# Optimization experiments

Measured on AMD Instinct MI355X. Metric: run time of the kernel, lower is better.

The kernel has to match this reference:

```python
import jax, jax.numpy as jnp
import numpy as np

T, X_D, M_N, CHUNK, REDUCE = 2048, 2048, 64, 64, 8
M_D = X_D // REDUCE          # 256
DECAY_D = M_D // 4           # 64
H_D = X_D * 2                # factor=2
FF_D = 256 * round(int(H_D * (2.0 / 3.0)) / 256)  # 2816


def setup_inputs() -> dict:
    key = jax.random.key(0)
    ks = jax.random.split(key, 20)
    def lin(k, out_d, in_d):
        return (jax.random.normal(k, (out_d, in_d), jnp.float32) / np.sqrt(in_d).astype(np.float32))
    return {
        "xs": jax.random.normal(ks[0], (T, X_D), jnp.float32),
        "attn_q": lin(ks[1], X_D // REDUCE, X_D),
        "attn_k": lin(ks[2], X_D // REDUCE, X_D // REDUCE),
        "attn_v": lin(ks[3], X_D, X_D),
        "attn_o": lin(ks[4], X_D, X_D),
        "attn_r": lin(ks[5], X_D, X_D),
        "mem_f": lin(ks[6], M_N, X_D),
        "mem_q": lin(ks[7], M_D, X_D),
        "mem_k": lin(ks[8], M_D, M_D),
        "mem_v": lin(ks[9], M_D, X_D),
        "mem_o": lin(ks[10], X_D, M_D),
        "mem_r": lin(ks[11], X_D, X_D),
        "mem_beta": -jnp.ones((M_N, M_D), jnp.float32),
        "mem_decay": 3.0 * jnp.ones((M_N, DECAY_D), jnp.float32),
        "mem_l": jax.random.uniform(ks[12], (M_N, M_D), dtype=jnp.float32),
        "ff_in1": lin(ks[13], FF_D, X_D),
        "ff_in2": lin(ks[14], FF_D, X_D),
        "ff_out": lin(ks[15], X_D, FF_D),
        "sn1_g": jnp.sqrt(jnp.float32(X_D)),
        "sn2_g": jnp.sqrt(jnp.float32(X_D)),
    }


def _rotate_half(x):
    x1 = x[..., ::2]
    x2 = x[..., 1::2]
    return jnp.stack((-x2, x1), axis=-1).reshape(x.shape)


def _scale_norm(x, g):
    return x * (g / (jnp.linalg.norm(x, axis=-1, keepdims=True) + 1e-8))


def _attn(xs, Wq, Wk, Wv, Wo, Wr):
    n = CHUNK
    q = xs @ Wq.T                       # (T, dk)
    k = q @ Wk.T                        # k is computed from q (as in source)
    v = xs @ Wv.T                       # (T, x_d)
    c = xs.shape[0] // n
    dk = q.shape[-1]
    q = q.reshape(c, n, dk)
    k = k.reshape(c, n, dk)
    v = v.reshape(c, n, v.shape[-1])

    def with_prev(a):                   # prepend previous chunk (zero for chunk 0)
        prev = jnp.concatenate([jnp.zeros_like(a[:1]), a[:-1]], axis=0)
        return jnp.concatenate([prev, a], axis=1)   # (c, 2n, d)

    k2, v2 = with_prev(k), with_prev(v)

    # RoPE over 2n key positions; queries take the last n positions
    inv_freq = 1.0 / (10000.0 ** (jnp.arange(0, dk, 2, dtype=jnp.float32) / dk))
    ang = jnp.arange(2 * n, dtype=jnp.float32)[:, None] * inv_freq[None, :]
    sin = jnp.repeat(jnp.sin(ang), 2, axis=-1)      # (2n, dk) interleaved
    cos = jnp.repeat(jnp.cos(ang), 2, axis=-1)
    q = q * cos[None, n:] + _rotate_half(q) * sin[None, n:]
    k2 = k2 * cos[None] + _rotate_half(k2) * sin[None]

    qk = jnp.einsum('cnk,cmk->cnm', q, k2) / jnp.sqrt(jnp.float32(dk))
    allowed = jnp.arange(2 * n)[None, :] <= (jnp.arange(n)[:, None] + n)  # tril offset n
    A = jax.nn.softmax(jnp.where(allowed[None], qk, -jnp.inf), axis=-1)
    y = jnp.einsum('cnm,cmv->cnv', A, v2).reshape(xs.shape[0], -1)
    return (y @ Wo.T) * jax.nn.sigmoid(xs @ Wr.T)


def _mem(xs, Wf, Wq, Wk, Wv, Wo, Wr, beta_p, decay_p, l_p):
    v = xs @ Wv.T                                       # (T, m_d)
    f = jax.nn.sigmoid(xs @ Wf.T)[:, :, None]           # (T, m_n, 1)
    beta = jax.nn.sigmoid(beta_p)[None]                 # (1, m_n, m_d)
    gamma = jnp.concatenate(
        [jnp.ones((M_N, M_D - DECAY_D), xs.dtype), jax.nn.sigmoid(decay_p)], axis=1
    )[None]                                             # (1, m_n, m_d)
    ws = (1.0 - f * beta) * gamma                       # (T, m_n, m_d)
    fvs = f * v[:, None, :]                             # (T, m_n, m_d)

    def bin_assoc(ei, ej):
        ai, bi = ei
        aj, bj = ej
        return (aj * ai, aj * bi + bj)

    _, mems = jax.lax.associative_scan(bin_assoc, (ws, fvs), axis=0)  # (T, m_n, m_d)

    q = xs @ Wq.T                                       # (T, m_d)
    k = jnp.einsum('nmd,kd->nmk', mems, Wk) + l_p[None]
    A = jax.nn.softmax(jnp.einsum('nmk,nk->nm', k, q) / jnp.sqrt(jnp.float32(M_D)), axis=-1)
    y = jnp.einsum('nm,nmd->nd', A, mems)
    return (y @ Wo.T) * jax.nn.sigmoid(xs @ Wr.T)


def _ff(xs, W1, W2, Wo):
    return (jax.nn.silu(xs @ W1.T) * (xs @ W2.T)) @ Wo.T


def reference(xs, attn_q, attn_k, attn_v, attn_o, attn_r,
              mem_f, mem_q, mem_k, mem_v, mem_o, mem_r,
              mem_beta, mem_decay, mem_l,
              ff_in1, ff_in2, ff_out, sn1_g, sn2_g):
    xn = _scale_norm(xs, sn1_g)
    xs = (_attn(xn, attn_q, attn_k, attn_v, attn_o, attn_r)
          + _mem(xn, mem_f, mem_q, mem_k, mem_v, mem_o, mem_r, mem_beta, mem_decay, mem_l)
          + xs)
    xs = _ff(_scale_norm(xs, sn2_g), ff_in1, ff_in2, ff_out) + xs
    return xs
```

## Files before the change

### kernel.cpp

```cpp
#include <hip/hip_runtime.h>
#include <math.h>


typedef short bhalf8 __attribute__((ext_vector_type(8)));
typedef float f32x4 __attribute__((ext_vector_type(4)));

#define CC_LD 7168
#define COL_V   0
#define COL_B1  2048
#define COL_B2  4096
#define COL_QB  6144
#define COL_VM  6400
#define COL_QM  6656
#define COL_FG  6912

#define AS1 __attribute__((address_space(1)))
#define AS3 __attribute__((address_space(3)))

__device__ __forceinline__ float sigmoidf_(float x){ return 1.0f/(1.0f+expf(-x)); }

__device__ __forceinline__ unsigned short f2b(float f){
  unsigned u = __float_as_uint(f);
  unsigned r = (u + 0x7fffu + ((u>>16)&1u)) >> 16;
  return (unsigned short)r;
}
__device__ __forceinline__ float b2f(unsigned short h){
  return __uint_as_float(((unsigned)h)<<16);
}

__global__ void k_f2b_all(
    const float* __restrict__ av, const float* __restrict__ ar, const float* __restrict__ mr,
    const float* __restrict__ aq, const float* __restrict__ mv, const float* __restrict__ mq,
    const float* __restrict__ mf, const float* __restrict__ ao, const float* __restrict__ mo,
    const float* __restrict__ f1, const float* __restrict__ f2, const float* __restrict__ fo,
    const float* __restrict__ ak,
    unsigned short* __restrict__ WCAT, unsigned short* __restrict__ AOB,
    unsigned short* __restrict__ MOB, unsigned short* __restrict__ FFW,
    unsigned short* __restrict__ FFOB, unsigned short* __restrict__ AKB){
  int i = blockIdx.x*256 + threadIdx.x;
  const float* s; unsigned short* d; int off;
  if (i < 3571712){
    d = WCAT + (size_t)i*4;
    if      (i < 1048576){ s = av; off = i; }
    else if (i < 2097152){ s = ar; off = i-1048576; }
    else if (i < 3145728){ s = mr; off = i-2097152; }
    else if (i < 3276800){ s = aq; off = i-3145728; }
    else if (i < 3407872){ s = mv; off = i-3276800; }
    else if (i < 3538944){ s = mq; off = i-3407872; }
    else                 { s = mf; off = i-3538944; }
  }
  else if (i < 4620288){ off = i-3571712; s = ao; d = AOB  + (size_t)off*4; }
  else if (i < 4751360){ off = i-4620288; s = mo; d = MOB  + (size_t)off*4; }
  else if (i < 6193152){ off = i-4751360; s = f1; d = FFW  + (size_t)off*4; }
  else if (i < 7634944){ off = i-6193152; s = f2; d = FFW  + (size_t)(off+1441792)*4; }
  else if (i < 9076736){ off = i-7634944; s = fo; d = FFOB + (size_t)off*4; }
  else if (i < 9093120){ off = i-9076736; s = ak; d = AKB  + (size_t)off*4; }
  else return;
  float4 v = ((const float4*)s)[off];
  ushort4 o;
  o.x = f2b(v.x); o.y = f2b(v.y); o.z = f2b(v.z); o.w = f2b(v.w);
  *(ushort4*)d = o;
}

__global__ void k_f2bT(const float* __restrict__ s, unsigned short* __restrict__ d){
  int i = blockIdx.x, j = threadIdx.x;
  d[(size_t)j*256 + i] = f2b(s[(size_t)i*256 + j]);
}

__global__ void k_trig(float2* __restrict__ TR){
  int idx = blockIdx.x*256 + threadIdx.x;
  int pos = idx >> 7, j = idx & 127;
  float inv = powf(10000.f, -(float)j/128.f);
  float a = (float)pos * inv;
  TR[idx] = make_float2(cosf(a), sinf(a));
}

__global__ __launch_bounds__(256) void k_scalenorm_b(const float* __restrict__ x,
    const float* __restrict__ g, unsigned short* __restrict__ ob){
  int row = blockIdx.x, tid = threadIdx.x;
  const float* xr = x + (size_t)row*2048;
  float ss = 0.f;
  for (int j = tid; j < 2048; j += 256){ float v = xr[j]; ss += v*v; }
  __shared__ float red[256];
  red[tid] = ss; __syncthreads();
  for (int s = 128; s > 0; s >>= 1){ if (tid < s) red[tid] += red[tid+s]; __syncthreads(); }
  float scale = g[0] / (sqrtf(red[0]) + 1e-8f);
  unsigned short* orow = ob + (size_t)row*2048;
  for (int j4 = tid; j4 < 512; j4 += 256){
    float4 v = *(const float4*)(xr + j4*4);
    ushort4 o;
    o.x = f2b(v.x*scale); o.y = f2b(v.y*scale); o.z = f2b(v.z*scale); o.w = f2b(v.w*scale);
    ((ushort4*)orow)[j4] = o;
  }
}

__global__ __launch_bounds__(256) void k_add3norm(const float* __restrict__ a,
    const float* __restrict__ b, const float* __restrict__ c,
    const float* __restrict__ g, float* __restrict__ xs2, unsigned short* __restrict__ xnb){
  int row = blockIdx.x, tid = threadIdx.x;
  size_t base = (size_t)row*512;
  float4 v[2]; float ss = 0.f;
#pragma unroll
  for (int i=0;i<2;++i){
    int j = tid + i*256;
    float4 x = ((const float4*)a)[base+j];
    float4 y = ((const float4*)b)[base+j];
    float4 z = ((const float4*)c)[base+j];
    float4 r; r.x=x.x+y.x+z.x; r.y=x.y+y.y+z.y; r.z=x.z+y.z+z.z; r.w=x.w+y.w+z.w;
    ((float4*)xs2)[base+j] = r;
    ss += r.x*r.x + r.y*r.y + r.z*r.z + r.w*r.w;
    v[i] = r;
  }
  __shared__ float red[256];
  red[tid] = ss; __syncthreads();
  for (int s = 128; s > 0; s >>= 1){ if (tid < s) red[tid] += red[tid+s]; __syncthreads(); }
  float scale = g[0] / (sqrtf(red[0]) + 1e-8f);
#pragma unroll
  for (int i=0;i<2;++i){
    int j = tid + i*256;
    ushort4 o;
    o.x = f2b(v[i].x*scale); o.y = f2b(v[i].y*scale);
    o.z = f2b(v[i].z*scale); o.w = f2b(v[i].w*scale);
    ((ushort4*)xnb)[base+j] = o;
  }
}

__global__ __launch_bounds__(256) void k_gemm_p(
    const unsigned short* __restrict__ A, int lda,
    const unsigned short* __restrict__ B,
    float* __restrict__ C, unsigned short* __restrict__ Cb,
    int N, int K, int ldc, int epi,
    const float* __restrict__ add,
    const unsigned short* __restrict__ gate, int gate_ld,
    const unsigned short* A2, const unsigned short* B2, float* C2){
  __shared__ unsigned short LDSu[24576];
  int tid = threadIdx.x;
  int w = tid >> 6, l = tid & 63;
  int bi = blockIdx.y, bj = blockIdx.x;
  const unsigned short* Ap = A; const unsigned short* Bp = B; float* Cp = C;
  if (blockIdx.z){ Ap = A2; Bp = B2; Cp = C2; }
  int m0 = bi*128, n0 = bj*128;
  int wr = w >> 1, wc = w & 1;

  f32x4 acc[4][4];
#pragma unroll
  for (int i=0;i<4;++i)
#pragma unroll
    for (int j=0;j<4;++j){ f32x4 z = {0.f,0.f,0.f,0.f}; acc[i][j] = z; }

  const int r0 = tid >> 2;
  const int gsrc8 = (((tid&3) ^ ((tid>>3)&3)) * 8);

  auto stage = [&](int bs, int kt){
    unsigned short* db = LDSu + bs*8192;
    const unsigned short* ap0 = Ap + (size_t)(m0 + r0)*lda      + kt*32 + gsrc8;
    const unsigned short* ap1 = Ap + (size_t)(m0 + 64 + r0)*lda + kt*32 + gsrc8;
    const unsigned short* bp0 = Bp + (size_t)(n0 + r0)*K        + kt*32 + gsrc8;
    const unsigned short* bp1 = Bp + (size_t)(n0 + 64 + r0)*K   + kt*32 + gsrc8;
    __builtin_amdgcn_global_load_lds((const AS1 void*)ap0, (AS3 void*)(db + tid*8),        16, 0, 0);
    __builtin_amdgcn_global_load_lds((const AS1 void*)ap1, (AS3 void*)(db + 2048 + tid*8), 16, 0, 0);
    __builtin_amdgcn_global_load_lds((const AS1 void*)bp0, (AS3 void*)(db + 4096 + tid*8), 16, 0, 0);
    __builtin_amdgcn_global_load_lds((const AS1 void*)bp1, (AS3 void*)(db + 6144 + tid*8), 16, 0, 0);
  };

  const int nt = K >> 5;
  stage(0, 0);
  stage(1, 1);
  asm volatile("s_waitcnt vmcnt(4)" ::: "memory");
  __builtin_amdgcn_s_barrier();

  const int lr = l & 15;
  const int gsw = (((l>>4) ^ ((l>>1)&3)) * 8);
  const int aoff = (wr*64 + lr)*32 + gsw;
  const int boff = 4096 + (wc*64 + lr)*32 + gsw;

  int cur = 0;
  for (int t = 0; t < nt; ++t){
    if (t + 2 < nt) stage((t+2)%3, t+2);
    const unsigned short* Tb = LDSu + cur*8192;
    bhalf8 af[4], bfr[4];
#pragma unroll
    for (int m=0;m<4;++m) af[m]  = *(const bhalf8*)(Tb + aoff + m*512);
#pragma unroll
    for (int n=0;n<4;++n) bfr[n] = *(const bhalf8*)(Tb + boff + n*512);
    __builtin_amdgcn_s_setprio(1);
#pragma unroll
    for (int m=0;m<4;++m)
#pragma unroll
      for (int n=0;n<4;++n)
        acc[m][n] = __builtin_amdgcn_mfma_f32_16x16x32_bf16(af[m], bfr[n], acc[m][n], 0, 0, 0);
    __builtin_amdgcn_s_setprio(0);
    if (t + 1 < nt){
      if (t + 2 < nt){ asm volatile("s_waitcnt vmcnt(4)" ::: "memory"); }
      else           { asm volatile("s_waitcnt vmcnt(0)" ::: "memory"); }
      __builtin_amdgcn_s_barrier();
      cur = (cur == 2) ? 0 : cur + 1;
    }
  }

#pragma unroll
  for (int m=0;m<4;++m){
    int rowb = m0 + wr*64 + m*16 + ((l>>4)<<2);
#pragma unroll
    for (int r=0;r<4;++r){
      int row = rowb + r;
      size_t rbase = (size_t)row*ldc;
      size_t gbase = (size_t)row*gate_ld;
#pragma unroll
      for (int n=0;n<4;++n){
        int col = n0 + wc*64 + n*16 + (l&15);
        float v = acc[m][n][r];
        if (add) v += add[rbase + col];
        if (epi == 2) v *= sigmoidf_(b2f(gate[gbase + col]));
        if (epi == 3) Cb[rbase + col] = f2b(v);
        else          Cp[rbase + col] = v;
      }
    }
  }
}

__global__ __launch_bounds__(256) void k_attn_scores_mfma(
    const unsigned short* __restrict__ CCqb, const float* __restrict__ K0,
    const float2* __restrict__ TR, unsigned short* __restrict__ P){
  __shared__ unsigned short Ks[128*256];
  int c = blockIdx.x, tid = threadIdx.x;
  for (int it = 0; it < 16; ++it){
    int id = tid + it*256;
    int m = id >> 5;
    int cs = (id & 31) * 8;
    float v[8];
    if (c == 0 && m < 64){
#pragma unroll
      for (int u=0;u<8;++u) v[u] = 0.f;
    } else {
      int gr = (c-1)*64 + m;
      const float* kr = K0 + (size_t)gr*256 + cs;
      float4 x0 = *(const float4*)kr, x1 = *(const float4*)(kr+4);
      v[0]=x0.x; v[1]=x0.y; v[2]=x0.z; v[3]=x0.w;
      v[4]=x1.x; v[5]=x1.y; v[6]=x1.z; v[7]=x1.w;
#pragma unroll
      for (int p2=0;p2<4;++p2){
        float2 t = TR[m*128 + (cs>>1) + p2];
        float e = v[2*p2], o = v[2*p2+1];
        v[2*p2]   = e*t.x - o*t.y;
        v[2*p2+1] = o*t.x + e*t.y;
      }
    }
    unsigned short pk[8];
#pragma unroll
    for (int u=0;u<8;++u) pk[u] = f2b(v[u]);
    int byte = m*512 + ((cs*2) ^ ((m&7)<<4));
    *(bhalf8*)((char*)&Ks[0] + byte) = *(const bhalf8*)pk;
  }
  __syncthreads();

  int w = tid >> 6, l = tid & 63;
  int lr = l & 15, lkg = l >> 4;
  f32x4 acc[8];
#pragma unroll
  for (int n=0;n<8;++n){ f32x4 z = {0.f,0.f,0.f,0.f}; acc[n] = z; }

  int iq = w*16 + lr;
  const unsigned short* qbase = CCqb + (size_t)(c*64 + iq)*CC_LD;
  int pos = 64 + iq;

  for (int kt = 0; kt < 8; ++kt){
    int k0c = kt*32 + lkg*8;
    bhalf8 q8 = *(const bhalf8*)(qbase + k0c);
    float v[8];
#pragma unroll
    for (int u=0;u<8;++u) v[u] = b2f((unsigned short)(((short*)&q8)[u]));
#pragma unroll
    for (int p2=0;p2<4;++p2){
      float2 t = TR[pos*128 + (k0c>>1) + p2];
      float e = v[2*p2], o = v[2*p2+1];
      v[2*p2]   = e*t.x - o*t.y;
      v[2*p2+1] = o*t.x + e*t.y;
    }
    unsigned short pk[8];
#pragma unroll
    for (int u=0;u<8;++u) pk[u] = f2b(v[u]);
    bhalf8 af = *(const bhalf8*)pk;
#pragma unroll
    for (int n=0;n<8;++n){
      int m = n*16 + lr;
      int byte = m*512 + ((k0c*2) ^ ((m&7)<<4));
      bhalf8 bf = *(const bhalf8*)((const char*)&Ks[0] + byte);
      acc[n] = __builtin_amdgcn_mfma_f32_16x16x32_bf16(af, bf, acc[n], 0, 0, 0);
    }
  }

  int i0 = w*16 + lkg*4;
  float mx[4] = {-1e30f,-1e30f,-1e30f,-1e30f};
  float sm[4] = {0.f,0.f,0.f,0.f};
#pragma unroll
  for (int n=0;n<8;++n){
    int col = n*16 + lr;
#pragma unroll
    for (int r=0;r<4;++r){
      float vv = acc[n][r] * (1.f/16.f);
      if (col > i0 + r + 64) vv = -1e30f;
      acc[n][r] = vv;
      mx[r] = fmaxf(mx[r], vv);
    }
  }
#pragma unroll
  for (int s=1; s<16; s<<=1)
#pragma unroll
    for (int r=0;r<4;++r) mx[r] = fmaxf(mx[r], __shfl_xor(mx[r], s));
#pragma unroll
  for (int n=0;n<8;++n)
#pragma unroll
    for (int r=0;r<4;++r){
      float e = expf(acc[n][r] - mx[r]);
      acc[n][r] = e; sm[r] += e;
    }
#pragma unroll
  for (int s=1; s<16; s<<=1)
#pragma unroll
    for (int r=0;r<4;++r) sm[r] += __shfl_xor(sm[r], s);
  float rcp[4];
#pragma unroll
  for (int r=0;r<4;++r) rcp[r] = 1.f/sm[r];

  unsigned short* Pr = P + (size_t)c*8192;
#pragma unroll
  for (int n=0;n<8;++n){
    int col = n*16 + lr;
#pragma unroll
    for (int r=0;r<4;++r)
      Pr[(i0+r)*128 + col] = f2b(acc[n][r]*rcp[r]);
  }
}

__global__ __launch_bounds__(256) void k_attn_pv_mfma(
    const unsigned short* __restrict__ P, const unsigned short* __restrict__ Vb, int vld,
    unsigned short* __restrict__ Y){
  __shared__ unsigned short Vt[128*128];
  int ct = blockIdx.x, c = blockIdx.y, tid = threadIdx.x;
  {
    int k = tid >> 1;
    int ch = (tid & 1) * 64;
    if (c == 0 && k < 64){
      for (int u=0; u<64; ++u){
        int col = ch + u;
        int byte = col*256 + ((k*2) ^ ((col&7)<<4));
        *(unsigned short*)((char*)&Vt[0] + byte) = 0;
      }
    } else {
      int gr = (c-1)*64 + k;
      const unsigned short* vr = Vb + (size_t)gr*vld + ct*128 + ch;
      for (int u8=0; u8<8; ++u8){
        bhalf8 x = *(const bhalf8*)(vr + u8*8);
#pragma unroll
        for (int u=0;u<8;++u){
          int col = ch + u8*8 + u;
          int byte = col*256 + ((k*2) ^ ((col&7)<<4));
          *(unsigned short*)((char*)&Vt[0] + byte) = (unsigned short)(((short*)&x)[u]);
        }
      }
    }
  }
  __syncthreads();
  int w = tid >> 6, l = tid & 63, lr = l & 15, lkg = l >> 4;
  f32x4 acc[8];
#pragma unroll
  for (int n=0;n<8;++n){ f32x4 z = {0.f,0.f,0.f,0.f}; acc[n] = z; }
  const unsigned short* Pr = P + (size_t)c*8192;
  for (int kt=0; kt<4; ++kt){
    int kb = kt*32 + lkg*8;
    bhalf8 af = *(const bhalf8*)(Pr + (w*16 + lr)*128 + kb);
#pragma unroll
    for (int n=0;n<8;++n){
      int col = n*16 + lr;
      int byte = col*256 + ((kb*2) ^ ((col&7)<<4));
      bhalf8 bf = *(const bhalf8*)((const char*)&Vt[0] + byte);
      acc[n] = __builtin_amdgcn_mfma_f32_16x16x32_bf16(af, bf, acc[n], 0, 0, 0);
    }
  }
  int row0 = c*64 + w*16 + lkg*4;
#pragma unroll
  for (int n=0;n<8;++n){
    int col = ct*128 + n*16 + lr;
#pragma unroll
    for (int r=0;r<4;++r)
      Y[(size_t)(row0+r)*2048 + col] = f2b(acc[n][r]);
  }
}

__global__ __launch_bounds__(256) void k_scan1(const unsigned short* __restrict__ CC,
    const float* __restrict__ beta_p, const float* __restrict__ decay_p,
    float* __restrict__ CP, float* __restrict__ CQ){
  int c = blockIdx.x, mg = blockIdx.y, d = threadIdx.x;
  __shared__ float Fs[512];
  for (int v = threadIdx.x; v < 512; v += 256){
    int s = v >> 3, j = v & 7;
    Fs[v] = sigmoidf_(b2f(CC[(size_t)(c*64+s)*CC_LD + COL_FG + mg*8 + j]));
  }
  __syncthreads();
  float beta[8], gamma[8], Pa[8], Qa[8];
#pragma unroll
  for (int j=0;j<8;++j){
    int m = mg*8+j;
    beta[j]  = sigmoidf_(beta_p[m*256+d]);
    gamma[j] = (d < 192) ? 1.f : sigmoidf_(decay_p[m*64 + (d-192)]);
    Pa[j] = 1.f; Qa[j] = 0.f;
  }
  for (int s = 0; s < 64; ++s){
    float vm = b2f(CC[(size_t)(c*64+s)*CC_LD + COL_VM + d]);
#pragma unroll
    for (int j=0;j<8;++j){
      float f = Fs[s*8+j];
      float w = (1.f - f*beta[j])*gamma[j];
      Pa[j] *= w;
      Qa[j] = w*Qa[j] + f*vm;
    }
  }
#pragma unroll
  for (int j=0;j<8;++j){
    size_t idx = ((size_t)c*64 + mg*8 + j)*256 + d;
    CP[idx] = Pa[j]; CQ[idx] = Qa[j];
  }
}

__global__ __launch_bounds__(256) void k_scan2(const float* __restrict__ CP,
    const float* __restrict__ CQ, float* __restrict__ SIN){
  int m = blockIdx.x, d = threadIdx.x;
  float S = 0.f;
  for (int c = 0; c < 32; ++c){
    size_t idx = ((size_t)c*64 + m)*256 + d;
    SIN[idx] = S;
    S = CP[idx]*S + CQ[idx];
  }
}

__global__ __launch_bounds__(256) void k_scan3(const unsigned short* __restrict__ CC,
    const float* __restrict__ beta_p, const float* __restrict__ decay_p,
    const float* __restrict__ SIN, unsigned short* __restrict__ MEMS){
  int c = blockIdx.x, mg = blockIdx.y, d = threadIdx.x;
  __shared__ float Fs[512];
  for (int v = threadIdx.x; v < 512; v += 256){
    int s = v >> 3, j = v & 7;
    Fs[v] = sigmoidf_(b2f(CC[(size_t)(c*64+s)*CC_LD + COL_FG + mg*8 + j]));
  }
  __syncthreads();
  float beta[8], gamma[8], S[8];
#pragma unroll
  for (int j=0;j<8;++j){
    int m = mg*8+j;
    beta[j]  = sigmoidf_(beta_p[m*256+d]);
    gamma[j] = (d < 192) ? 1.f : sigmoidf_(decay_p[m*64 + (d-192)]);
    S[j] = SIN[((size_t)c*64 + m)*256 + d];
  }
  for (int s = 0; s < 64; ++s){
    float vm = b2f(CC[(size_t)(c*64+s)*CC_LD + COL_VM + d]);
    size_t tb = (size_t)(c*64+s)*64;
#pragma unroll
    for (int j=0;j<8;++j){
      float f = Fs[s*8+j];
      float w = (1.f - f*beta[j])*gamma[j];
      S[j] = w*S[j] + f*vm;
      MEMS[(tb + mg*8 + j)*256 + d] = f2b(S[j]);
    }
  }
}

__global__ __launch_bounds__(256) void k_memread(const unsigned short* __restrict__ MEMS,
    const float* __restrict__ QH, const unsigned short* __restrict__ QMs, int qm_ld,
    const float* __restrict__ L, unsigned short* __restrict__ YMb){
  int t = blockIdx.x, tid = threadIdx.x;
  int wave = tid >> 6, lane = tid & 63;
  __shared__ float anorm[64];
  const unsigned short* Mt = MEMS + (size_t)t*16384;
  float4 qh4 = *(const float4*)(QH + (size_t)t*256 + lane*4);
  ushort4 qmu = *(const ushort4*)(QMs + (size_t)t*qm_ld + lane*4);
  float qm0 = b2f(qmu.x), qm1 = b2f(qmu.y), qm2 = b2f(qmu.z), qm3 = b2f(qmu.w);
  for (int mi = 0; mi < 16; ++mi){
    int m = wave*16 + mi;
    ushort4 su = *(const ushort4*)(Mt + m*256 + lane*4);
    float4 l4 = *(const float4*)(L + (size_t)m*256 + lane*4);
    float p = b2f(su.x)*qh4.x + b2f(su.y)*qh4.y + b2f(su.z)*qh4.z + b2f(su.w)*qh4.w
            + l4.x*qm0 + l4.y*qm1 + l4.z*qm2 + l4.w*qm3;
#pragma unroll
    for (int off = 32; off > 0; off >>= 1) p += __shfl_down(p, off);
    if (lane == 0) anorm[m] = p * (1.f/16.f);
  }
  __syncthreads();
  if (tid == 0){
    float mx = -INFINITY;
    for (int i = 0; i < 64; ++i) mx = fmaxf(mx, anorm[i]);
    float sum = 0.f;
    for (int i = 0; i < 64; ++i){ float e = expf(anorm[i]-mx); anorm[i] = e; sum += e; }
    float r = 1.f/sum;
    for (int i = 0; i < 64; ++i) anorm[i] *= r;
  }
  __syncthreads();
  float acc = 0.f;
  for (int m = 0; m < 64; ++m) acc += anorm[m]*b2f(Mt[m*256 + tid]);
  YMb[(size_t)t*256 + tid] = f2b(acc);
}

__global__ void k_silumul_b2(const unsigned short* __restrict__ H12b,
                             unsigned short* __restrict__ H1b, int n4){
  int i = blockIdx.x*256 + threadIdx.x;
  if (i < n4){
    int r = i / 704, c4 = i % 704;
    ushort4 a4 = *(const ushort4*)(H12b + (size_t)r*5632 + c4*4);
    ushort4 b4 = *(const ushort4*)(H12b + (size_t)r*5632 + 2816 + c4*4);
    float ax = b2f(a4.x), ay = b2f(a4.y), az = b2f(a4.z), aw = b2f(a4.w);
    ushort4 o;
    o.x = f2b(ax*sigmoidf_(ax)*b2f(b4.x));
    o.y = f2b(ay*sigmoidf_(ay)*b2f(b4.y));
    o.z = f2b(az*sigmoidf_(az)*b2f(b4.z));
    o.w = f2b(aw*sigmoidf_(aw)*b2f(b4.w));
    ((ushort4*)H1b)[i] = o;
  }
}

extern "C" void kernel_launch(void* const* d_in, const int* in_sizes, int n_in,
                              void* d_out, int out_size, void* d_ws, size_t ws_size,
                              hipStream_t stream){
  const float* xs        = (const float*)d_in[0];
  const float* attn_q    = (const float*)d_in[1];
  const float* attn_k    = (const float*)d_in[2];
  const float* attn_v    = (const float*)d_in[3];
  const float* attn_o    = (const float*)d_in[4];
  const float* attn_r    = (const float*)d_in[5];
  const float* mem_f     = (const float*)d_in[6];
  const float* mem_q     = (const float*)d_in[7];
  const float* mem_k     = (const float*)d_in[8];
  const float* mem_v     = (const float*)d_in[9];
  const float* mem_o     = (const float*)d_in[10];
  const float* mem_r     = (const float*)d_in[11];
  const float* mem_beta  = (const float*)d_in[12];
  const float* mem_decay = (const float*)d_in[13];
  const float* mem_l     = (const float*)d_in[14];
  const float* ff1       = (const float*)d_in[15];
  const float* ff2       = (const float*)d_in[16];
  const float* ffo       = (const float*)d_in[17];
  const float* sn1       = (const float*)d_in[18];
  const float* sn2       = (const float*)d_in[19];
  float* out = (float*)d_out;
  float* W = (float*)d_ws;

  unsigned short* XNb  = (unsigned short*)(W + 0);
  unsigned short* WCAT = (unsigned short*)(W + 2097152);
  unsigned short* CCb  = (unsigned short*)(W + 9437184);
  unsigned short* AOB  = (unsigned short*)(W + 16777216);
  unsigned short* MOB  = (unsigned short*)(W + 18874368);
  unsigned short* FFW  = (unsigned short*)(W + 19136512);
  unsigned short* FFOB = (unsigned short*)(W + 24903680);
  unsigned short* AKB  = (unsigned short*)(W + 27787264);
  unsigned short* MKTB = (unsigned short*)(W + 27820032);
  unsigned short* Ybb  = (unsigned short*)(W + 27852800);
  float*          B2f  = W + 29949952;
  float*          XS2  = W + 34144256;
  unsigned short* MEMSb= (unsigned short*)(W + 38338560);
  float*          CP   = W + 55115776;
  float*          CQ   = W + 55640064;
  float*          SIN  = W + 56164352;
  float2*         TRIG = (float2*)(W + 0);
  float*          K0   = W + 32768;
  unsigned short* P    = (unsigned short*)(W + 557056);
  float*          QH   = W + 688128;
  unsigned short* YMb  = (unsigned short*)(W + 1212416);
  float*          B1f  = W + 2097152;
  unsigned short* XN2b = MEMSb;
  unsigned short* H1b  = (unsigned short*)(W + 40435712);
  unsigned short* H12b = CCb;

  dim3 blk(256);

  k_f2b_all<<<dim3(35520), blk, 0, stream>>>(attn_v, attn_r, mem_r, attn_q, mem_v, mem_q,
      mem_f, attn_o, mem_o, ff1, ff2, ffo, attn_k, WCAT, AOB, MOB, FFW, FFOB, AKB);
  hipMemsetAsync(WCAT + 14286848, 0, 786432, stream);
  k_f2bT<<<dim3(256), blk, 0, stream>>>(mem_k, MKTB);

  k_scalenorm_b<<<dim3(2048), blk, 0, stream>>>(xs, sn1, XNb);

  k_gemm_p<<<dim3(56, 16), blk, 0, stream>>>(XNb, 2048, WCAT, nullptr, CCb, CC_LD, 2048, CC_LD, 3,
      nullptr, nullptr, 0, nullptr, nullptr, nullptr);

  k_trig<<<dim3(64), blk, 0, stream>>>(TRIG);

  k_gemm_p<<<dim3(2, 16, 2), blk, 0, stream>>>(CCb + COL_QB, CC_LD, AKB, K0, nullptr, 256, 256, 256, 0,
      nullptr, nullptr, 0, CCb + COL_QM, MKTB, QH);

  k_attn_scores_mfma<<<dim3(32), blk, 0, stream>>>(CCb + COL_QB, K0, TRIG, P);
  k_attn_pv_mfma<<<dim3(16, 32), blk, 0, stream>>>(P, CCb + COL_V, CC_LD, Ybb);
  k_gemm_p<<<dim3(16, 16), blk, 0, stream>>>(Ybb, 2048, AOB, B1f, nullptr, 2048, 2048, 2048, 2,
      nullptr, CCb + COL_B1, CC_LD, nullptr, nullptr, nullptr);

  k_scan1<<<dim3(32, 8), blk, 0, stream>>>(CCb, mem_beta, mem_decay, CP, CQ);
  k_scan2<<<dim3(64), blk, 0, stream>>>(CP, CQ, SIN);
  k_scan3<<<dim3(32, 8), blk, 0, stream>>>(CCb, mem_beta, mem_decay, SIN, MEMSb);
  k_memread<<<dim3(2048), blk, 0, stream>>>(MEMSb, QH, CCb + COL_QM, CC_LD, mem_l, YMb);
  k_gemm_p<<<dim3(16, 16), blk, 0, stream>>>(YMb, 256, MOB, B2f, nullptr, 2048, 256, 2048, 2,
      nullptr, CCb + COL_B2, CC_LD, nullptr, nullptr, nullptr);

  k_add3norm<<<dim3(2048), blk, 0, stream>>>(B1f, B2f, xs, sn2, XS2, XN2b);

  k_gemm_p<<<dim3(44, 16), blk, 0, stream>>>(XN2b, 2048, FFW, nullptr, H12b, 5632, 2048, 5632, 3,
      nullptr, nullptr, 0, nullptr, nullptr, nullptr);
  k_silumul_b2<<<dim3(5632), blk, 0, stream>>>(H12b, H1b, 1441792);
  k_gemm_p<<<dim3(16, 16), blk, 0, stream>>>(H1b, 2816, FFOB, out, nullptr, 2048, 2816, 2048, 0,
      XS2, nullptr, 0, nullptr, nullptr, nullptr);
}
```

Baseline: 457.3 us.

## Fuse attn/mem output GEMMs with residual; fuse SwiGLU into FF GEMM epilogue

The attention-output and memory-output GEMMs now run as two K-loops inside one kernel, which applies both sigmoid gates and the residual add directly. This removes the B1f/B2f fp32 intermediates and the add3norm pass, which is replaced by a plain scalenorm on XS2. The ff_in1 and ff_in2 weight rows are interleaved so each adjacent column pair of the FF-in GEMM holds the matching h1/h2 values. A shuffle in the epilogue then writes silu(h1)*h2 directly, removing the H12 buffer and the separate silumul kernel. The memread softmax moves from a serial single-thread loop to wave shuffles; the fused GEMM adds register pressure from its second accumulator set.

```diff
diff --git a/kernel.cpp b/kernel.cpp
--- a/kernel.cpp
+++ b/kernel.cpp
@@ -51,8 +51,12 @@
   }
   else if (i < 4620288){ off = i-3571712; s = ao; d = AOB  + (size_t)off*4; }
   else if (i < 4751360){ off = i-4620288; s = mo; d = MOB  + (size_t)off*4; }
-  else if (i < 6193152){ off = i-4751360; s = f1; d = FFW  + (size_t)off*4; }
-  else if (i < 7634944){ off = i-6193152; s = f2; d = FFW  + (size_t)(off+1441792)*4; }
+  else if (i < 6193152){ off = i-4751360; s = f1;
+    int row = off >> 9, c4 = off & 511;
+    d = FFW + ((size_t)row*2)*2048 + c4*4; }
+  else if (i < 7634944){ off = i-6193152; s = f2;
+    int row = off >> 9, c4 = off & 511;
+    d = FFW + ((size_t)row*2 + 1)*2048 + c4*4; }
   else if (i < 9076736){ off = i-7634944; s = fo; d = FFOB + (size_t)off*4; }
   else if (i < 9093120){ off = i-9076736; s = ak; d = AKB  + (size_t)off*4; }
   else return;
@@ -94,37 +98,6 @@
   }
 }
 
-__global__ __launch_bounds__(256) void k_add3norm(const float* __restrict__ a,
-    const float* __restrict__ b, const float* __restrict__ c,
-    const float* __restrict__ g, float* __restrict__ xs2, unsigned short* __restrict__ xnb){
-  int row = blockIdx.x, tid = threadIdx.x;
-  size_t base = (size_t)row*512;
-  float4 v[2]; float ss = 0.f;
-#pragma unroll
-  for (int i=0;i<2;++i){
-    int j = tid + i*256;
-    float4 x = ((const float4*)a)[base+j];
-    float4 y = ((const float4*)b)[base+j];
-    float4 z = ((const float4*)c)[base+j];
-    float4 r; r.x=x.x+y.x+z.x; r.y=x.y+y.y+z.y; r.z=x.z+y.z+z.z; r.w=x.w+y.w+z.w;
-    ((float4*)xs2)[base+j] = r;
-    ss += r.x*r.x + r.y*r.y + r.z*r.z + r.w*r.w;
-    v[i] = r;
-  }
-  __shared__ float red[256];
-  red[tid] = ss; __syncthreads();
-  for (int s = 128; s > 0; s >>= 1){ if (tid < s) red[tid] += red[tid+s]; __syncthreads(); }
-  float scale = g[0] / (sqrtf(red[0]) + 1e-8f);
-#pragma unroll
-  for (int i=0;i<2;++i){
-    int j = tid + i*256;
-    ushort4 o;
-    o.x = f2b(v[i].x*scale); o.y = f2b(v[i].y*scale);
-    o.z = f2b(v[i].z*scale); o.w = f2b(v[i].w*scale);
-    ((ushort4*)xnb)[base+j] = o;
-  }
-}
-
 __global__ __launch_bounds__(256) void k_gemm_p(
     const unsigned short* __restrict__ A, int lda,
     const unsigned short* __restrict__ B,
@@ -210,10 +183,138 @@
       for (int n=0;n<4;++n){
         int col = n0 + wc*64 + n*16 + (l&15);
         float v = acc[m][n][r];
+        if (epi == 4){
+          float o = __shfl_xor(v, 1);
+          if ((l & 1) == 0)
+            Cb[gbase + (col>>1)] = f2b(v*sigmoidf_(v)*o);
+          continue;
+        }
         if (add) v += add[rbase + col];
         if (epi == 2) v *= sigmoidf_(b2f(gate[gbase + col]));
         if (epi == 3) Cb[rbase + col] = f2b(v);
         else          Cp[rbase + col] = v;
+      }
+    }
+  }
+}
+
+__global__ __launch_bounds__(256) void k_gemm_fuse2(
+    const unsigned short* __restrict__ A,  const unsigned short* __restrict__ B,
+    const unsigned short* __restrict__ A2, const unsigned short* __restrict__ B2,
+    const unsigned short* __restrict__ gate1, const unsigned short* __restrict__ gate2,
+    const float* __restrict__ xs, float* __restrict__ XS2){
+  __shared__ unsigned short LDSu[24576];
+  int tid = threadIdx.x;
+  int w = tid >> 6, l = tid & 63;
+  int bi = blockIdx.y, bj = blockIdx.x;
+  int m0 = bi*128, n0 = bj*128;
+  int wr = w >> 1, wc = w & 1;
+
+  f32x4 acc[4][4], acc2[4][4];
+#pragma unroll
+  for (int i=0;i<4;++i)
+#pragma unroll
+    for (int j=0;j<4;++j){ f32x4 z = {0.f,0.f,0.f,0.f}; acc[i][j] = z; acc2[i][j] = z; }
+
+  const int r0 = tid >> 2;
+  const int gsrc8 = (((tid&3) ^ ((tid>>3)&3)) * 8);
+
+  auto stage = [&](int bs, int kt, const unsigned short* Ap, int lda,
+                   const unsigned short* Bp, int ldb){
+    unsigned short* db = LDSu + bs*8192;
+    const unsigned short* ap0 = Ap + (size_t)(m0 + r0)*lda      + kt*32 + gsrc8;
+    const unsigned short* ap1 = Ap + (size_t)(m0 + 64 + r0)*lda + kt*32 + gsrc8;
+    const unsigned short* bp0 = Bp + (size_t)(n0 + r0)*ldb      + kt*32 + gsrc8;
+    const unsigned short* bp1 = Bp + (size_t)(n0 + 64 + r0)*ldb + kt*32 + gsrc8;
+    __builtin_amdgcn_global_load_lds((const AS1 void*)ap0, (AS3 void*)(db + tid*8),        16, 0, 0);
+    __builtin_amdgcn_global_load_lds((const AS1 void*)ap1, (AS3 void*)(db + 2048 + tid*8), 16, 0, 0);
+    __builtin_amdgcn_global_load_lds((const AS1 void*)bp0, (AS3 void*)(db + 4096 + tid*8), 16, 0, 0);
+    __builtin_amdgcn_global_load_lds((const AS1 void*)bp1, (AS3 void*)(db + 6144 + tid*8), 16, 0, 0);
+  };
+
+  const int lr = l & 15;
+  const int gsw = (((l>>4) ^ ((l>>1)&3)) * 8);
+  const int aoff = (wr*64 + lr)*32 + gsw;
+  const int boff = 4096 + (wc*64 + lr)*32 + gsw;
+
+  {
+    const int nt = 64;
+    stage(0, 0, A, 2048, B, 2048);
+    stage(1, 1, A, 2048, B, 2048);
+    asm volatile("s_waitcnt vmcnt(4)" ::: "memory");
+    __builtin_amdgcn_s_barrier();
+    int cur = 0;
+    for (int t = 0; t < nt; ++t){
+      if (t + 2 < nt) stage((t+2)%3, t+2, A, 2048, B, 2048);
+      const unsigned short* Tb = LDSu + cur*8192;
+      bhalf8 af[4], bfr[4];
+#pragma unroll
+      for (int m=0;m<4;++m) af[m]  = *(const bhalf8*)(Tb + aoff + m*512);
+#pragma unroll
+      for (int n=0;n<4;++n) bfr[n] = *(const bhalf8*)(Tb + boff + n*512);
+      __builtin_amdgcn_s_setprio(1);
+#pragma unroll
+      for (int m=0;m<4;++m)
+#pragma unroll
+        for (int n=0;n<4;++n)
+          acc[m][n] = __builtin_amdgcn_mfma_f32_16x16x32_bf16(af[m], bfr[n], acc[m][n], 0, 0, 0);
+      __builtin_amdgcn_s_setprio(0);
+      if (t + 1 < nt){
+        if (t + 2 < nt){ asm volatile("s_waitcnt vmcnt(4)" ::: "memory"); }
+        else           { asm volatile("s_waitcnt vmcnt(0)" ::: "memory"); }
+        __builtin_amdgcn_s_barrier();
+        cur = (cur == 2) ? 0 : cur + 1;
+      }
+    }
+  }
+  __syncthreads();
+
+  {
+    const int nt = 8;
+    stage(0, 0, A2, 256, B2, 256);
+    stage(1, 1, A2, 256, B2, 256);
+    asm volatile("s_waitcnt vmcnt(4)" ::: "memory");
+    __builtin_amdgcn_s_barrier();
+    int cur = 0;
+    for (int t = 0; t < nt; ++t){
+      if (t + 2 < nt) stage((t+2)%3, t+2, A2, 256, B2, 256);
+      const unsigned short* Tb = LDSu + cur*8192;
+      bhalf8 af[4], bfr[4];
+#pragma unroll
+      for (int m=0;m<4;++m) af[m]  = *(const bhalf8*)(Tb + aoff + m*512);
+#pragma unroll
+      for (int n=0;n<4;++n) bfr[n] = *(const bhalf8*)(Tb + boff + n*512);
+      __builtin_amdgcn_s_setprio(1);
+#pragma unroll
+      for (int m=0;m<4;++m)
+#pragma unroll
+        for (int n=0;n<4;++n)
+          acc2[m][n] = __builtin_amdgcn_mfma_f32_16x16x32_bf16(af[m], bfr[n], acc2[m][n], 0, 0, 0);
+      __builtin_amdgcn_s_setprio(0);
+      if (t + 1 < nt){
+        if (t + 2 < nt){ asm volatile("s_waitcnt vmcnt(4)" ::: "memory"); }
+        else           { asm volatile("s_waitcnt vmcnt(0)" ::: "memory"); }
+        __builtin_amdgcn_s_barrier();
+        cur = (cur == 2) ? 0 : cur + 1;
+      }
+    }
+  }
+
+#pragma unroll
+  for (int m=0;m<4;++m){
+    int rowb = m0 + wr*64 + m*16 + ((l>>4)<<2);
+#pragma unroll
+    for (int r=0;r<4;++r){
+      int row = rowb + r;
+      size_t gb = (size_t)row*CC_LD;
+      size_t rb = (size_t)row*2048;
+#pragma unroll
+      for (int n=0;n<4;++n){
+        int col = n0 + wc*64 + n*16 + (l&15);
+        float v = acc[m][n][r]*sigmoidf_(b2f(gate1[gb + col]))
+                + acc2[m][n][r]*sigmoidf_(b2f(gate2[gb + col]))
+                + xs[rb + col];
+        XS2[rb + col] = v;
       }
     }
   }
@@ -486,35 +587,21 @@
     if (lane == 0) anorm[m] = p * (1.f/16.f);
   }
   __syncthreads();
-  if (tid == 0){
-    float mx = -INFINITY;
-    for (int i = 0; i < 64; ++i) mx = fmaxf(mx, anorm[i]);
-    float sum = 0.f;
-    for (int i = 0; i < 64; ++i){ float e = expf(anorm[i]-mx); anorm[i] = e; sum += e; }
-    float r = 1.f/sum;
-    for (int i = 0; i < 64; ++i) anorm[i] *= r;
+  if (tid < 64){
+    float v = anorm[tid];
+    float mx = v;
+#pragma unroll
+    for (int off = 32; off > 0; off >>= 1) mx = fmaxf(mx, __shfl_xor(mx, off));
+    float e = expf(v - mx);
+    float s = e;
+#pragma unroll
+    for (int off = 32; off > 0; off >>= 1) s += __shfl_xor(s, off);
+    anorm[tid] = e / s;
   }
   __syncthreads();
   float acc = 0.f;
   for (int m = 0; m < 64; ++m) acc += anorm[m]*b2f(Mt[m*256 + tid]);
   YMb[(size_t)t*256 + tid] = f2b(acc);
-}
-
-__global__ void k_silumul_b2(const unsigned short* __restrict__ H12b,
-                             unsigned short* __restrict__ H1b, int n4){
-  int i = blockIdx.x*256 + threadIdx.x;
-  if (i < n4){
-    int r = i / 704, c4 = i % 704;
-    ushort4 a4 = *(const ushort4*)(H12b + (size_t)r*5632 + c4*4);
-    ushort4 b4 = *(const ushort4*)(H12b + (size_t)r*5632 + 2816 + c4*4);
-    float ax = b2f(a4.x), ay = b2f(a4.y), az = b2f(a4.z), aw = b2f(a4.w);
-    ushort4 o;
-    o.x = f2b(ax*sigmoidf_(ax)*b2f(b4.x));
-    o.y = f2b(ay*sigmoidf_(ay)*b2f(b4.y));
-    o.z = f2b(az*sigmoidf_(az)*b2f(b4.z));
-    o.w = f2b(aw*sigmoidf_(aw)*b2f(b4.w));
-    ((ushort4*)H1b)[i] = o;
-  }
 }
 
 extern "C" void kernel_launch(void* const* d_in, const int* in_sizes, int n_in,
@@ -553,7 +640,6 @@
   unsigned short* AKB  = (unsigned short*)(W + 27787264);
   unsigned short* MKTB = (unsigned short*)(W + 27820032);
   unsigned short* Ybb  = (unsigned short*)(W + 27852800);
-  float*          B2f  = W + 29949952;
   float*          XS2  = W + 34144256;
   unsigned short* MEMSb= (unsigned short*)(W + 38338560);
   float*          CP   = W + 55115776;
@@ -564,16 +650,13 @@
   unsigned short* P    = (unsigned short*)(W + 557056);
   float*          QH   = W + 688128;
   unsigned short* YMb  = (unsigned short*)(W + 1212416);
-  float*          B1f  = W + 2097152;
   unsigned short* XN2b = MEMSb;
   unsigned short* H1b  = (unsigned short*)(W + 40435712);
-  unsigned short* H12b = CCb;
 
   dim3 blk(256);
 
   k_f2b_all<<<dim3(35520), blk, 0, stream>>>(attn_v, attn_r, mem_r, attn_q, mem_v, mem_q,
       mem_f, attn_o, mem_o, ff1, ff2, ffo, attn_k, WCAT, AOB, MOB, FFW, FFOB, AKB);
-  hipMemsetAsync(WCAT + 14286848, 0, 786432, stream);
   k_f2bT<<<dim3(256), blk, 0, stream>>>(mem_k, MKTB);
 
   k_scalenorm_b<<<dim3(2048), blk, 0, stream>>>(xs, sn1, XNb);
@@ -588,21 +671,19 @@
 
   k_attn_scores_mfma<<<dim3(32), blk, 0, stream>>>(CCb + COL_QB, K0, TRIG, P);
   k_attn_pv_mfma<<<dim3(16, 32), blk, 0, stream>>>(P, CCb + COL_V, CC_LD, Ybb);
-  k_gemm_p<<<dim3(16, 16), blk, 0, stream>>>(Ybb, 2048, AOB, B1f, nullptr, 2048, 2048, 2048, 2,
-      nullptr, CCb + COL_B1, CC_LD, nullptr, nullptr, nullptr);
 
   k_scan1<<<dim3(32, 8), blk, 0, stream>>>(CCb, mem_beta, mem_decay, CP, CQ);
   k_scan2<<<dim3(64), blk, 0, stream>>>(CP, CQ, SIN);
   k_scan3<<<dim3(32, 8), blk, 0, stream>>>(CCb, mem_beta, mem_decay, SIN, MEMSb);
   k_memread<<<dim3(2048), blk, 0, stream>>>(MEMSb, QH, CCb + COL_QM, CC_LD, mem_l, YMb);
-  k_gemm_p<<<dim3(16, 16), blk, 0, stream>>>(YMb, 256, MOB, B2f, nullptr, 2048, 256, 2048, 2,
-      nullptr, CCb + COL_B2, CC_LD, nullptr, nullptr, nullptr);
-
-  k_add3norm<<<dim3(2048), blk, 0, stream>>>(B1f, B2f, xs, sn2, XS2, XN2b);
-
-  k_gemm_p<<<dim3(44, 16), blk, 0, stream>>>(XN2b, 2048, FFW, nullptr, H12b, 5632, 2048, 5632, 3,
-      nullptr, nullptr, 0, nullptr, nullptr, nullptr);
-  k_silumul_b2<<<dim3(5632), blk, 0, stream>>>(H12b, H1b, 1441792);
+
+  k_gemm_fuse2<<<dim3(16, 16), blk, 0, stream>>>(Ybb, AOB, YMb, MOB,
+      CCb + COL_B1, CCb + COL_B2, xs, XS2);
+
+  k_scalenorm_b<<<dim3(2048), blk, 0, stream>>>(XS2, sn2, XN2b);
+
+  k_gemm_p<<<dim3(44, 16), blk, 0, stream>>>(XN2b, 2048, FFW, nullptr, H1b, 5632, 2048, 5632, 4,
+      nullptr, nullptr, 2816, nullptr, nullptr, nullptr);
   k_gemm_p<<<dim3(16, 16), blk, 0, stream>>>(H1b, 2816, FFOB, out, nullptr, 2048, 2816, 2048, 0,
       XS2, nullptr, 0, nullptr, nullptr, nullptr);
 }
```

Result: faster. 416.5 us (-8.9%).
